# Kernel optimization log

Hardware: AMD Instinct MI355X
Metric: run time of the kernel (lower is better)

The kernel has to match this reference:

```python
import jax, jax.numpy as jnp
import numpy as np

DIM, HEADS, DHEAD = 256, 8, 64
HID = HEADS * DHEAD


def _elu1(x):
    # F.elu(x) + 1 == exp(x) for x<0, x+1 for x>=0
    return jnp.where(x > 0, x + 1.0, jnp.exp(x))


def setup_inputs() -> dict:
    key = jax.random.key(0)
    ks = jax.random.split(key, 6)
    B, H, W = 8, 64, 64
    x = jax.random.normal(ks[0], (B, DIM, H, W), dtype=jnp.float32)
    contact_map = jax.random.uniform(ks[1], (B, 1, H, W), dtype=jnp.float32)
    s_qkv = 1.0 / np.sqrt(DIM)
    Wqkv = jax.random.normal(ks[2], (3 * HID, DIM), dtype=jnp.float32) * s_qkv
    s_out = 1.0 / np.sqrt(HID)
    Wout = jax.random.normal(ks[3], (DIM, HID), dtype=jnp.float32) * s_out
    bout = jax.random.normal(ks[4], (DIM,), dtype=jnp.float32) * 0.01
    contact_scale = jnp.float32(0.1)
    return {"x": x, "contact_map": contact_map, "Wqkv": Wqkv,
            "Wout": Wout, "bout": bout, "contact_scale": contact_scale}


def reference(x, contact_map, Wqkv, Wout, bout, contact_scale):
    b, c, h, w = x.shape
    n = h * w
    xf = x.reshape(b, c, n)                                  # b c n
    qkv = jnp.einsum('oc,bcn->bon', Wqkv, xf)                # b (3*H*D) n
    qkv = qkv.reshape(b, 3, HEADS, DHEAD, n)                 # qkv-major channel order
    q = _elu1(qkv[:, 0])                                     # b h d n
    k = _elu1(qkv[:, 1])
    v = qkv[:, 2]
    cm = contact_map.reshape(b, 1, 1, n)                     # b 1 1 n
    k = k * (1.0 + contact_scale * cm)
    kv = jnp.einsum('bhdn,bhen->bhde', k, v)                 # b h d e
    ksum = k.sum(axis=-1)                                    # b h d
    z = 1.0 / (jnp.einsum('bhdn,bhd->bhn', q, ksum) + 1e-6)  # b h n
    out = jnp.einsum('bhde,bhdn->bhne', kv, q) * z[..., None]  # b h n e
    out = out.transpose(0, 1, 3, 2).reshape(b, HID, n)       # b (h d) n
    y = jnp.einsum('oc,bcn->bon', Wout, out) + bout[None, :, None]
    return y.reshape(b, -1, h, w)
```

## Files before the change

### kernel.cpp

```cpp
#include <hip/hip_runtime.h>
#include <stdint.h>


#define NPIX 4096
#define HIDC 512
#define DIMC 256
#define BATCH 8

typedef __attribute__((ext_vector_type(8))) short bf16x8;
typedef __attribute__((ext_vector_type(4))) float f32x4;
typedef __attribute__((ext_vector_type(16))) float f32x16;

__device__ __forceinline__ float bf2f(unsigned short h) {
    unsigned int u = ((unsigned int)h) << 16; float f;
    __builtin_memcpy(&f, &u, 4); return f;
}
__device__ __forceinline__ unsigned short f2bf(float f) {
    unsigned int u; __builtin_memcpy(&u, &f, 4);
    u += 0x7fffu + ((u >> 16) & 1u);
    return (unsigned short)(u >> 16);
}
__device__ __forceinline__ float elu1(float x) {
    return x > 0.f ? x + 1.f : __expf(x);
}
__device__ __forceinline__ void gl16(const unsigned short* g, unsigned short* l) {
    __builtin_amdgcn_global_load_lds(
        (__attribute__((address_space(1))) const void*)g,
        (__attribute__((address_space(3))) void*)l, 16, 0, 0);
}

__global__ __launch_bounds__(256) void k_convW(
    const float* __restrict__ Wqkv, const float* __restrict__ Wout,
    unsigned short* __restrict__ Wb, unsigned short* __restrict__ Wob)
{
    int i4 = (blockIdx.x * 256 + threadIdx.x) * 4;
    const int NW1 = 1536 * 256;
    float4 v; unsigned short* dst;
    if (i4 < NW1) { v = *(const float4*)&Wqkv[i4]; dst = Wb + i4; }
    else { int j = i4 - NW1; v = *(const float4*)&Wout[j]; dst = Wob + j; }
    ushort4 o; o.x = f2bf(v.x); o.y = f2bf(v.y); o.z = f2bf(v.z); o.w = f2bf(v.w);
    *(ushort4*)dst = o;
}

__global__ __launch_bounds__(256) void k_tx(
    const float* __restrict__ x, unsigned short* __restrict__ xT)
{
    __shared__ float tile[32][33];
    const int n0 = blockIdx.x * 32, c0 = blockIdx.y * 32, b = blockIdx.z;
    const int t = threadIdx.x;
    const int r = t >> 3, c4 = (t & 7) * 4;
    float4 v = *(const float4*)&x[((size_t)b * DIMC + c0 + r) * NPIX + n0 + c4];
    tile[r][c4 + 0] = v.x; tile[r][c4 + 1] = v.y;
    tile[r][c4 + 2] = v.z; tile[r][c4 + 3] = v.w;
    __syncthreads();
    ushort4 o;
    unsigned short* op = (unsigned short*)&o;
#pragma unroll
    for (int i = 0; i < 4; i++) op[i] = f2bf(tile[c4 + i][r]);
    *(ushort4*)&xT[((size_t)b * NPIX + n0 + r) * DIMC + c0 + c4] = o;
}

__global__ __launch_bounds__(256) void k_fused(
    const unsigned short* __restrict__ xT,
    const unsigned short* __restrict__ Wb,
    const float* __restrict__ cmp,
    const float* __restrict__ csp,
    unsigned short* __restrict__ qT,
    float* __restrict__ kvq,
    float* __restrict__ ksump)
{
    const int b  = blockIdx.z;
    const int m0 = blockIdx.x * 128;
    const int yb = blockIdx.y;
    const int h  = yb - 4;
    const int t = threadIdx.x;
    const int wave = t >> 6, lane = t & 63;
    const int wm = wave >> 1, wn = wave & 1;
    const int l31 = lane & 31, lhi = lane >> 5;

    __shared__ unsigned short sh[128 * 128];
    unsigned short* As  = sh;
    unsigned short* Bs  = sh + 128 * 64;
    unsigned short* kvS = sh;

    const unsigned short* Ag = xT + ((size_t)b * NPIX + m0) * DIMC;

    f32x16 acc[2][2];
#pragma unroll
    for (int i = 0; i < 2; i++)
#pragma unroll
        for (int j = 0; j < 2; j++)
#pragma unroll
            for (int r = 0; r < 16; r++) acc[i][j][r] = 0.f;

    const int r8  = lane >> 3;
    const int jg8 = (((lane & 7) ^ r8) & 7) * 8;
    const int xsw = (l31 & 7);

    for (int k0 = 0; k0 < DIMC; k0 += 64) {
#pragma unroll
        for (int i = 0; i < 4; i++) {
            const int rowg = wave * 32 + i * 8;
            const int arow = rowg + r8;
            gl16(&Ag[(size_t)arow * DIMC + k0 + jg8], &As[rowg * 64]);
            int wrow;
            if (yb < 4) wrow = yb * 128 + arow;
            else wrow = (arow < 64) ? (512 + h * 64 + arow)
                                    : (1024 + h * 64 + (arow - 64));
            gl16(&Wb[(size_t)wrow * DIMC + k0 + jg8], &Bs[rowg * 64]);
        }
        __syncthreads();
#pragma unroll
        for (int ks = 0; ks < 4; ks++) {
            const int coff = ((ks * 2 + lhi) ^ xsw) * 8;
            bf16x8 af[2], bfg[2];
#pragma unroll
            for (int fm = 0; fm < 2; fm++)
                af[fm] = *(const bf16x8*)&As[(wm * 64 + fm * 32 + l31) * 64 + coff];
#pragma unroll
            for (int fn = 0; fn < 2; fn++)
                bfg[fn] = *(const bf16x8*)&Bs[(wn * 64 + fn * 32 + l31) * 64 + coff];
#pragma unroll
            for (int fm = 0; fm < 2; fm++)
#pragma unroll
                for (int fn = 0; fn < 2; fn++)
                    acc[fm][fn] = __builtin_amdgcn_mfma_f32_32x32x16_bf16(
                        af[fm], bfg[fn], acc[fm][fn], 0, 0, 0);
        }
        __syncthreads();
    }

    if (yb < 4) {
        const int n0 = yb * 128;
#pragma unroll
        for (int fm = 0; fm < 2; fm++) {
            const int pbase = m0 + wm * 64 + fm * 32;
#pragma unroll
            for (int fn = 0; fn < 2; fn++) {
                const int o = n0 + wn * 64 + fn * 32 + l31;
#pragma unroll
                for (int r = 0; r < 16; r++) {
                    int prow = pbase + (r & 3) + 8 * (r >> 2) + 4 * lhi;
                    qT[((size_t)b * NPIX + prow) * HIDC + o] = f2bf(elu1(acc[fm][fn][r]));
                }
            }
        }
        return;
    }

    const float cs = *csp;
    const bool isK = (wn == 0);
    float gv4[2];
#pragma unroll
    for (int fm = 0; fm < 2; fm++)
        gv4[fm] = 1.f + cs * cmp[(size_t)b * NPIX + m0 + wm * 64 + fm * 32 + l31];

    float gk[2][16];
#pragma unroll
    for (int fm = 0; fm < 2; fm++)
#pragma unroll
        for (int r = 0; r < 16; r++)
            gk[fm][r] = __shfl(gv4[fm], (r & 3) + 8 * (r >> 2) + 4 * lhi);

    float ks0 = 0.f, ks1 = 0.f;
#pragma unroll
    for (int fm = 0; fm < 2; fm++) {
#pragma unroll
        for (int fn = 0; fn < 2; fn++) {
            const int o = wn * 64 + fn * 32 + l31;
            const int sw = (o & 7) << 3;
#pragma unroll
            for (int rg = 0; rg < 4; rg++) {
                ushort4 pk4;
                unsigned short* pp = (unsigned short*)&pk4;
#pragma unroll
                for (int j = 0; j < 4; j++) {
                    const int r = rg * 4 + j;
                    float val = acc[fm][fn][r];
                    if (isK) {
                        float kvl = elu1(val) * gk[fm][r];
                        if (fn == 0) ks0 += kvl; else ks1 += kvl;
                        pp[j] = f2bf(kvl);
                    } else {
                        pp[j] = f2bf(val);
                    }
                }
                const int px0 = wm * 64 + fm * 32 + rg * 8 + 4 * lhi;
                *(ushort4*)&kvS[(size_t)o * 128 + (px0 ^ sw)] = pk4;
            }
        }
    }
    if (isK) {
        atomicAdd(&ksump[(size_t)(b * 8 + h) * 64 + l31], ks0);
        atomicAdd(&ksump[(size_t)(b * 8 + h) * 64 + 32 + l31], ks1);
    }
    __syncthreads();

    f32x16 kva;
#pragma unroll
    for (int r = 0; r < 16; r++) kva[r] = 0.f;
#pragma unroll
    for (int pk = 0; pk < 8; pk++) {
        const int co = ((pk * 2 + lhi) ^ (l31 & 7)) * 8;
        bf16x8 kf = *(const bf16x8*)&kvS[(size_t)(wm * 32 + l31) * 128 + co];
        bf16x8 vf = *(const bf16x8*)&kvS[(size_t)(64 + wn * 32 + l31) * 128 + co];
        kva = __builtin_amdgcn_mfma_f32_32x32x16_bf16(kf, vf, kva, 0, 0, 0);
    }
    float* kvb = kvq + ((size_t)(b * 8 + h) * 32 + blockIdx.x) * 4096;
#pragma unroll
    for (int r = 0; r < 16; r++) {
        const int d = wm * 32 + (r & 3) + 8 * (r >> 2) + 4 * lhi;
        kvb[(size_t)d * 64 + wn * 32 + l31] = kva[r];
    }
}

__global__ __launch_bounds__(256) void k_kvred(
    const float* __restrict__ kvq, float* __restrict__ kvp)
{
    const int bh = blockIdx.x >> 2, q4 = blockIdx.x & 3;
    const float4* src = (const float4*)(kvq + (size_t)bh * 32 * 4096)
                      + q4 * 256 + threadIdx.x;
    float4 s; s.x = 0.f; s.y = 0.f; s.z = 0.f; s.w = 0.f;
#pragma unroll 8
    for (int i = 0; i < 32; i++) {
        float4 v = src[(size_t)i * 1024];
        s.x += v.x; s.y += v.y; s.z += v.z; s.w += v.w;
    }
    ((float4*)(kvp + (size_t)bh * 4096))[q4 * 256 + threadIdx.x] = s;
}

#define LS3 72
__global__ __launch_bounds__(256) void k_out(
    const unsigned short* __restrict__ qT,
    const float* __restrict__ kv, const float* __restrict__ ksum,
    unsigned short* __restrict__ outT)
{
    const int bh = blockIdx.y, p0 = blockIdx.x * 128;
    const int b = bh >> 3, h = bh & 7;
    const int t = threadIdx.x, wave = t >> 6, lane = t & 63;
    const int l31 = lane & 31, lhi = lane >> 5;

    __shared__ unsigned short Aq[128 * LS3];
    __shared__ unsigned short Bv[96 * LS3];

    const unsigned short* qg = qT + ((size_t)b * NPIX + p0) * HIDC + h * 64;
#pragma unroll
    for (int i = 0; i < 4; i++) {
        int idx = t + i * 256;
        int row = idx >> 3, c8 = (idx & 7) * 8;
        *(uint4*)&Aq[row * LS3 + c8] = *(const uint4*)&qg[(size_t)row * HIDC + c8];
    }
    const float* kvg = kv + (size_t)bh * 4096;
#pragma unroll
    for (int i = 0; i < 16; i++) {
        int idx = t + i * 256;
        int d = idx >> 6, e = idx & 63;
        Bv[e * LS3 + d] = f2bf(kvg[idx]);
    }
    if (t < 64) {
        float ksv = ksum[bh * 64 + t];
        unsigned short hi = f2bf(ksv);
        Bv[64 * LS3 + t] = hi;
        Bv[65 * LS3 + t] = f2bf(ksv - bf2f(hi));
    }
    for (int i = t; i < 30 * 64; i += 256)
        Bv[(66 + (i >> 6)) * LS3 + (i & 63)] = 0;
    __syncthreads();

    f32x16 acc[3];
#pragma unroll
    for (int j = 0; j < 3; j++)
#pragma unroll
        for (int r = 0; r < 16; r++) acc[j][r] = 0.f;

#pragma unroll
    for (int ksub = 0; ksub < 4; ksub++) {
        const int koff = ksub * 16 + lhi * 8;
        bf16x8 af = *(const bf16x8*)&Aq[(wave * 32 + l31) * LS3 + koff];
#pragma unroll
        for (int nf = 0; nf < 3; nf++) {
            bf16x8 bfg = *(const bf16x8*)&Bv[(nf * 32 + l31) * LS3 + koff];
            acc[nf] = __builtin_amdgcn_mfma_f32_32x32x16_bf16(af, bfg, acc[nf], 0, 0, 0);
        }
    }

    unsigned short* og = outT + ((size_t)b * NPIX + p0 + wave * 32) * HIDC + h * 64;
#pragma unroll
    for (int r = 0; r < 16; r++) {
        float hi = __shfl(acc[2][r], lane & 32);
        float lo = __shfl(acc[2][r], (lane & 32) | 1);
        float z = 1.f / (hi + lo + 1e-6f);
        int prow = (r & 3) + 8 * (r >> 2) + 4 * lhi;
#pragma unroll
        for (int nf = 0; nf < 2; nf++)
            og[(size_t)prow * HIDC + nf * 32 + l31] = f2bf(acc[nf][r] * z);
    }
}

__global__ __launch_bounds__(256) void k_y(
    const unsigned short* __restrict__ outT,
    const unsigned short* __restrict__ Wob,
    const float* __restrict__ bout,
    float* __restrict__ y)
{
    const int b  = blockIdx.z;
    const int m0 = blockIdx.x * 128;
    const int n0 = blockIdx.y * 128;
    const int t = threadIdx.x;
    const int wave = t >> 6, lane = t & 63;
    const int wm = wave >> 1, wn = wave & 1;
    const int lrow = lane & 15, quad = lane >> 4;

    __shared__ unsigned short As[128 * 64];
    __shared__ unsigned short Bs[128 * 64];

    const unsigned short* Ag = outT + ((size_t)b * NPIX + m0) * HIDC;
    const unsigned short* Bg = Wob + (size_t)n0 * HIDC;

    f32x4 acc[4][4];
#pragma unroll
    for (int i = 0; i < 4; i++)
#pragma unroll
        for (int j = 0; j < 4; j++) acc[i][j] = (f32x4){0.f, 0.f, 0.f, 0.f};

    const int r8  = lane >> 3;
    const int jg8 = (((lane & 7) ^ r8) & 7) * 8;
    const int xswA = (lrow & 7);

    for (int k0 = 0; k0 < HIDC; k0 += 64) {
#pragma unroll
        for (int i = 0; i < 4; i++) {
            const int rowg = wave * 32 + i * 8;
            gl16(&Ag[(size_t)(rowg + r8) * HIDC + k0 + jg8], &As[rowg * 64]);
            gl16(&Bg[(size_t)(rowg + r8) * HIDC + k0 + jg8], &Bs[rowg * 64]);
        }
        __syncthreads();
#pragma unroll
        for (int ksb = 0; ksb < 2; ksb++) {
            bf16x8 af[4], bfr[4];
#pragma unroll
            for (int mt = 0; mt < 4; mt++) {
                const int row = wm * 64 + mt * 16 + lrow;
                af[mt] = *(const bf16x8*)&As[row * 64 + (((ksb * 4 + quad) ^ xswA)) * 8];
            }
#pragma unroll
            for (int nt = 0; nt < 4; nt++) {
                const int row = wn * 64 + nt * 16 + lrow;
                bfr[nt] = *(const bf16x8*)&Bs[row * 64 + (((ksb * 4 + quad) ^ xswA)) * 8];
            }
#pragma unroll
            for (int mt = 0; mt < 4; mt++)
#pragma unroll
                for (int nt = 0; nt < 4; nt++)
                    acc[mt][nt] = __builtin_amdgcn_mfma_f32_16x16x32_bf16(
                        af[mt], bfr[nt], acc[mt][nt], 0, 0, 0);
        }
        __syncthreads();
    }

#pragma unroll
    for (int mt = 0; mt < 4; mt++) {
        const int pixel0 = m0 + wm * 64 + mt * 16 + quad * 4;
#pragma unroll
        for (int nt = 0; nt < 4; nt++) {
            const int o = n0 + wn * 64 + nt * 16 + lrow;
            const float bias = bout[o];
            f32x4 a = acc[mt][nt];
            float4 st; st.x = a[0] + bias; st.y = a[1] + bias;
            st.z = a[2] + bias; st.w = a[3] + bias;
            *(float4*)&y[((size_t)b * DIMC + o) * NPIX + pixel0] = st;
        }
    }
}

extern "C" void kernel_launch(void* const* d_in, const int* in_sizes, int n_in,
                              void* d_out, int out_size, void* d_ws, size_t ws_size,
                              hipStream_t stream) {
    (void)in_sizes; (void)n_in; (void)out_size; (void)ws_size;
    const float* x    = (const float*)d_in[0];
    const float* cm   = (const float*)d_in[1];
    const float* Wqkv = (const float*)d_in[2];
    const float* Wout = (const float*)d_in[3];
    const float* bout = (const float*)d_in[4];
    const float* csp  = (const float*)d_in[5];
    float* y = (float*)d_out;

    const size_t qn = (size_t)BATCH * HIDC * NPIX;
    char* ws = (char*)d_ws;
    unsigned short* qT   = (unsigned short*)ws;                 ws += qn * 2;
    unsigned short* outT = (unsigned short*)ws;                 ws += qn * 2;
    unsigned short* xT   = outT;
    float* kvp   = (float*)ws;                                  ws += (size_t)64 * 64 * 64 * 4;
    float* ksump = (float*)ws;                                  ws += (size_t)64 * 64 * 4;
    float* kvq   = (float*)ws;                                  ws += (size_t)64 * 32 * 4096 * 4;
    unsigned short* Wb  = (unsigned short*)ws;                  ws += (size_t)1536 * 256 * 2;
    unsigned short* Wob = (unsigned short*)ws;

    hipMemsetAsync(ksump, 0, (size_t)64 * 64 * sizeof(float), stream);
    k_convW<<<512, 256, 0, stream>>>(Wqkv, Wout, Wb, Wob);
    k_tx   <<<dim3(128, 8, 8), 256, 0, stream>>>(x, xT);
    k_fused<<<dim3(32, 12, 8), 256, 0, stream>>>(xT, Wb, cm, csp, qT, kvq, ksump);
    k_kvred<<<256, 256, 0, stream>>>(kvq, kvp);
    k_out  <<<dim3(32, 64),    256, 0, stream>>>(qT, kvp, ksump, outT);
    k_y    <<<dim3(32, 2, 8),  256, 0, stream>>>(outT, Wob, bout, y);
}
```

Before: 210.1 us.

## Fuse per-head output attention and output projection into one kernel

```diff
diff --git a/kernel.cpp b/kernel.cpp
--- a/kernel.cpp
+++ b/kernel.cpp
@@ -31,15 +31,23 @@
 
 __global__ __launch_bounds__(256) void k_convW(
     const float* __restrict__ Wqkv, const float* __restrict__ Wout,
-    unsigned short* __restrict__ Wb, unsigned short* __restrict__ Wob)
+    unsigned short* __restrict__ Wb, unsigned short* __restrict__ Wpo)
 {
     int i4 = (blockIdx.x * 256 + threadIdx.x) * 4;
     const int NW1 = 1536 * 256;
-    float4 v; unsigned short* dst;
-    if (i4 < NW1) { v = *(const float4*)&Wqkv[i4]; dst = Wb + i4; }
-    else { int j = i4 - NW1; v = *(const float4*)&Wout[j]; dst = Wob + j; }
-    ushort4 o; o.x = f2bf(v.x); o.y = f2bf(v.y); o.z = f2bf(v.z); o.w = f2bf(v.w);
-    *(ushort4*)dst = o;
+    if (i4 < NW1) {
+        float4 v = *(const float4*)&Wqkv[i4];
+        ushort4 u; u.x = f2bf(v.x); u.y = f2bf(v.y); u.z = f2bf(v.z); u.w = f2bf(v.w);
+        *(ushort4*)&Wb[i4] = u;
+    } else {
+        int jj = i4 - NW1;
+        float4 v = *(const float4*)&Wout[jj];
+        ushort4 u; u.x = f2bf(v.x); u.y = f2bf(v.y); u.z = f2bf(v.z); u.w = f2bf(v.w);
+        const int o = jj >> 9, c = jj & 511;
+        const int og = o >> 5, l31 = o & 31;
+        const int ks = c >> 4, lhi = (c >> 3) & 1, j = c & 7;
+        *(ushort4*)&Wpo[og * 16384 + ks * 512 + (l31 * 2 + lhi) * 8 + j] = u;
+    }
 }
 
 __global__ __launch_bounds__(256) void k_tx(
@@ -229,146 +237,132 @@
     ((float4*)(kvp + (size_t)bh * 4096))[q4 * 256 + threadIdx.x] = s;
 }
 
-#define LS3 72
-__global__ __launch_bounds__(256) void k_out(
+__global__ __launch_bounds__(256, 2) void k_oy(
     const unsigned short* __restrict__ qT,
-    const float* __restrict__ kv, const float* __restrict__ ksum,
-    unsigned short* __restrict__ outT)
-{
-    const int bh = blockIdx.y, p0 = blockIdx.x * 128;
-    const int b = bh >> 3, h = bh & 7;
-    const int t = threadIdx.x, wave = t >> 6, lane = t & 63;
-    const int l31 = lane & 31, lhi = lane >> 5;
-
-    __shared__ unsigned short Aq[128 * LS3];
-    __shared__ unsigned short Bv[96 * LS3];
-
-    const unsigned short* qg = qT + ((size_t)b * NPIX + p0) * HIDC + h * 64;
-#pragma unroll
-    for (int i = 0; i < 4; i++) {
-        int idx = t + i * 256;
-        int row = idx >> 3, c8 = (idx & 7) * 8;
-        *(uint4*)&Aq[row * LS3 + c8] = *(const uint4*)&qg[(size_t)row * HIDC + c8];
-    }
-    const float* kvg = kv + (size_t)bh * 4096;
-#pragma unroll
-    for (int i = 0; i < 16; i++) {
-        int idx = t + i * 256;
-        int d = idx >> 6, e = idx & 63;
-        Bv[e * LS3 + d] = f2bf(kvg[idx]);
-    }
-    if (t < 64) {
-        float ksv = ksum[bh * 64 + t];
-        unsigned short hi = f2bf(ksv);
-        Bv[64 * LS3 + t] = hi;
-        Bv[65 * LS3 + t] = f2bf(ksv - bf2f(hi));
-    }
-    for (int i = t; i < 30 * 64; i += 256)
-        Bv[(66 + (i >> 6)) * LS3 + (i & 63)] = 0;
-    __syncthreads();
-
-    f32x16 acc[3];
-#pragma unroll
-    for (int j = 0; j < 3; j++)
-#pragma unroll
-        for (int r = 0; r < 16; r++) acc[j][r] = 0.f;
-
-#pragma unroll
-    for (int ksub = 0; ksub < 4; ksub++) {
-        const int koff = ksub * 16 + lhi * 8;
-        bf16x8 af = *(const bf16x8*)&Aq[(wave * 32 + l31) * LS3 + koff];
-#pragma unroll
-        for (int nf = 0; nf < 3; nf++) {
-            bf16x8 bfg = *(const bf16x8*)&Bv[(nf * 32 + l31) * LS3 + koff];
-            acc[nf] = __builtin_amdgcn_mfma_f32_32x32x16_bf16(af, bfg, acc[nf], 0, 0, 0);
-        }
-    }
-
-    unsigned short* og = outT + ((size_t)b * NPIX + p0 + wave * 32) * HIDC + h * 64;
-#pragma unroll
-    for (int r = 0; r < 16; r++) {
-        float hi = __shfl(acc[2][r], lane & 32);
-        float lo = __shfl(acc[2][r], (lane & 32) | 1);
-        float z = 1.f / (hi + lo + 1e-6f);
-        int prow = (r & 3) + 8 * (r >> 2) + 4 * lhi;
-#pragma unroll
-        for (int nf = 0; nf < 2; nf++)
-            og[(size_t)prow * HIDC + nf * 32 + l31] = f2bf(acc[nf][r] * z);
-    }
-}
-
-__global__ __launch_bounds__(256) void k_y(
-    const unsigned short* __restrict__ outT,
-    const unsigned short* __restrict__ Wob,
+    const float* __restrict__ kvp,
+    const float* __restrict__ ksum,
+    const unsigned short* __restrict__ Wpo,
     const float* __restrict__ bout,
     float* __restrict__ y)
 {
-    const int b  = blockIdx.z;
-    const int m0 = blockIdx.x * 128;
-    const int n0 = blockIdx.y * 128;
+    const int b  = blockIdx.y;
+    const int px0 = blockIdx.x * 64;
     const int t = threadIdx.x;
     const int wave = t >> 6, lane = t & 63;
-    const int wm = wave >> 1, wn = wave & 1;
-    const int lrow = lane & 15, quad = lane >> 4;
-
-    __shared__ unsigned short As[128 * 64];
-    __shared__ unsigned short Bs[128 * 64];
-
-    const unsigned short* Ag = outT + ((size_t)b * NPIX + m0) * HIDC;
-    const unsigned short* Bg = Wob + (size_t)n0 * HIDC;
-
-    f32x4 acc[4][4];
-#pragma unroll
-    for (int i = 0; i < 4; i++)
-#pragma unroll
-        for (int j = 0; j < 4; j++) acc[i][j] = (f32x4){0.f, 0.f, 0.f, 0.f};
-
-    const int r8  = lane >> 3;
-    const int jg8 = (((lane & 7) ^ r8) & 7) * 8;
-    const int xswA = (lrow & 7);
-
-    for (int k0 = 0; k0 < HIDC; k0 += 64) {
-#pragma unroll
-        for (int i = 0; i < 4; i++) {
-            const int rowg = wave * 32 + i * 8;
-            gl16(&Ag[(size_t)(rowg + r8) * HIDC + k0 + jg8], &As[rowg * 64]);
-            gl16(&Bg[(size_t)(rowg + r8) * HIDC + k0 + jg8], &Bs[rowg * 64]);
-        }
+    const int pxh = wave & 1, whi = wave >> 1;
+    const int l31 = lane & 31, lhi = lane >> 5;
+    const int lidx = (l31 * 2 + lhi) * 8;
+
+    __shared__ unsigned short qS[2][64 * 64];
+    __shared__ unsigned short kvS2[64 * 72];
+    __shared__ unsigned short outS[64 * 64];
+    __shared__ float ksS[64];
+
+    const int r8 = lane >> 3;
+    const int jg8 = ((lane & 7) ^ r8) * 8;
+
+    auto stageQ = [&](int h, int buf) {
+        const unsigned short* qg = qT + ((size_t)b * NPIX + px0) * HIDC + h * 64;
+#pragma unroll
+        for (int i = 0; i < 2; i++) {
+            const int rowb = wave * 16 + i * 8;
+            gl16(&qg[(size_t)(rowb + r8) * HIDC + jg8], &qS[buf][rowb * 64]);
+        }
+    };
+    auto stageKV = [&](int h) {
+        const float* kvg = kvp + (size_t)(b * 8 + h) * 4096;
+#pragma unroll
+        for (int i = 0; i < 16; i++) {
+            int idx = t + i * 256;
+            int d = idx >> 6, e = idx & 63;
+            kvS2[e * 72 + d] = f2bf(kvg[idx]);
+        }
+        if (t < 64) ksS[t] = ksum[(size_t)(b * 8 + h) * 64 + t];
+    };
+
+    stageQ(0, 0);
+    stageKV(0);
+
+    f32x16 yacc[4];
+#pragma unroll
+    for (int mt = 0; mt < 4; mt++)
+#pragma unroll
+        for (int r = 0; r < 16; r++) yacc[mt][r] = 0.f;
+
+    int cur = 0;
+    __syncthreads();
+
+#pragma unroll 1
+    for (int h = 0; h < 8; h++) {
+        bf16x8 qf[4];
+#pragma unroll
+        for (int s = 0; s < 4; s++)
+            qf[s] = *(const bf16x8*)&qS[cur][(pxh * 32 + l31) * 64
+                                            + (((s * 2 + lhi) ^ (l31 & 7)) * 8)];
+        f32x16 oacc;
+#pragma unroll
+        for (int r = 0; r < 16; r++) oacc[r] = 0.f;
+#pragma unroll
+        for (int s = 0; s < 4; s++) {
+            bf16x8 kvf = *(const bf16x8*)&kvS2[(whi * 32 + l31) * 72 + s * 16 + lhi * 8];
+            oacc = __builtin_amdgcn_mfma_f32_32x32x16_bf16(kvf, qf[s], oacc, 0, 0, 0);
+        }
+        float den = 0.f;
+#pragma unroll
+        for (int s = 0; s < 4; s++) {
+            f32x4 ka = *(const f32x4*)&ksS[s * 16 + lhi * 8];
+            f32x4 kb = *(const f32x4*)&ksS[s * 16 + lhi * 8 + 4];
+            const unsigned short* qp = (const unsigned short*)&qf[s];
+#pragma unroll
+            for (int j = 0; j < 4; j++) {
+                den += bf2f(qp[j]) * ka[j];
+                den += bf2f(qp[4 + j]) * kb[j];
+            }
+        }
+        den += __shfl_xor(den, 32);
+        const float z = 1.f / (den + 1e-6f);
+
+        ushort4 op4[4];
+#pragma unroll
+        for (int rg = 0; rg < 4; rg++) {
+            unsigned short* pp = (unsigned short*)&op4[rg];
+#pragma unroll
+            for (int j = 0; j < 4; j++)
+                pp[j] = f2bf(oacc[rg * 4 + j] * z);
+        }
+
         __syncthreads();
-#pragma unroll
-        for (int ksb = 0; ksb < 2; ksb++) {
-            bf16x8 af[4], bfr[4];
+        {
+            const int px = pxh * 32 + l31;
+#pragma unroll
+            for (int rg = 0; rg < 4; rg++)
+                *(ushort4*)&outS[px * 64 + (((whi * 4 + rg) ^ (px & 7)) * 8) + 4 * lhi]
+                    = op4[rg];
+        }
+        if (h < 7) { stageQ(h + 1, cur ^ 1); stageKV(h + 1); }
+        __syncthreads();
+
+#pragma unroll
+        for (int k16 = 0; k16 < 4; k16++) {
+            const int px = pxh * 32 + l31;
+            bf16x8 of = *(const bf16x8*)&outS[px * 64 + (((k16 * 2 + lhi) ^ (px & 7)) * 8)];
 #pragma unroll
             for (int mt = 0; mt < 4; mt++) {
-                const int row = wm * 64 + mt * 16 + lrow;
-                af[mt] = *(const bf16x8*)&As[row * 64 + (((ksb * 4 + quad) ^ xswA)) * 8];
+                bf16x8 wf = *(const bf16x8*)&Wpo[(size_t)(whi * 4 + mt) * 16384
+                                                 + (h * 4 + k16) * 512 + lidx];
+                yacc[mt] = __builtin_amdgcn_mfma_f32_32x32x16_bf16(wf, of, yacc[mt], 0, 0, 0);
             }
-#pragma unroll
-            for (int nt = 0; nt < 4; nt++) {
-                const int row = wn * 64 + nt * 16 + lrow;
-                bfr[nt] = *(const bf16x8*)&Bs[row * 64 + (((ksb * 4 + quad) ^ xswA)) * 8];
-            }
-#pragma unroll
-            for (int mt = 0; mt < 4; mt++)
-#pragma unroll
-                for (int nt = 0; nt < 4; nt++)
-                    acc[mt][nt] = __builtin_amdgcn_mfma_f32_16x16x32_bf16(
-                        af[mt], bfr[nt], acc[mt][nt], 0, 0, 0);
-        }
-        __syncthreads();
+        }
+        cur ^= 1;
     }
 
 #pragma unroll
     for (int mt = 0; mt < 4; mt++) {
-        const int pixel0 = m0 + wm * 64 + mt * 16 + quad * 4;
-#pragma unroll
-        for (int nt = 0; nt < 4; nt++) {
-            const int o = n0 + wn * 64 + nt * 16 + lrow;
-            const float bias = bout[o];
-            f32x4 a = acc[mt][nt];
-            float4 st; st.x = a[0] + bias; st.y = a[1] + bias;
-            st.z = a[2] + bias; st.w = a[3] + bias;
-            *(float4*)&y[((size_t)b * DIMC + o) * NPIX + pixel0] = st;
+#pragma unroll
+        for (int r = 0; r < 16; r++) {
+            const int o = whi * 128 + mt * 32 + (r & 3) + 8 * (r >> 2) + 4 * lhi;
+            y[((size_t)b * DIMC + o) * NPIX + px0 + pxh * 32 + l31]
+                = yacc[mt][r] + bout[o];
         }
     }
 }
@@ -388,19 +382,17 @@
     const size_t qn = (size_t)BATCH * HIDC * NPIX;
     char* ws = (char*)d_ws;
     unsigned short* qT   = (unsigned short*)ws;                 ws += qn * 2;
-    unsigned short* outT = (unsigned short*)ws;                 ws += qn * 2;
-    unsigned short* xT   = outT;
+    unsigned short* xT   = (unsigned short*)ws;                 ws += qn * 2;
     float* kvp   = (float*)ws;                                  ws += (size_t)64 * 64 * 64 * 4;
     float* ksump = (float*)ws;                                  ws += (size_t)64 * 64 * 4;
     float* kvq   = (float*)ws;                                  ws += (size_t)64 * 32 * 4096 * 4;
     unsigned short* Wb  = (unsigned short*)ws;                  ws += (size_t)1536 * 256 * 2;
-    unsigned short* Wob = (unsigned short*)ws;
+    unsigned short* Wpo = (unsigned short*)ws;
 
     hipMemsetAsync(ksump, 0, (size_t)64 * 64 * sizeof(float), stream);
-    k_convW<<<512, 256, 0, stream>>>(Wqkv, Wout, Wb, Wob);
+    k_convW<<<512, 256, 0, stream>>>(Wqkv, Wout, Wb, Wpo);
     k_tx   <<<dim3(128, 8, 8), 256, 0, stream>>>(x, xT);
     k_fused<<<dim3(32, 12, 8), 256, 0, stream>>>(xT, Wb, cm, csp, qT, kvq, ksump);
     k_kvred<<<256, 256, 0, stream>>>(kvq, kvp);
-    k_out  <<<dim3(32, 64),    256, 0, stream>>>(qT, kvp, ksump, outT);
-    k_y    <<<dim3(32, 2, 8),  256, 0, stream>>>(outT, Wob, bout, y);
-}
+    k_oy   <<<dim3(64, 8),     256, 0, stream>>>(qT, kvp, ksump, Wpo, bout, y);
+}
```

Result: faster. 199.9 us (-4.9%).
